# Performance work log

Measured on AMD Instinct MI355X. Metric: run time of the kernel, lower is better.

The kernel has to match this reference:

```python
import jax, jax.numpy as jnp
import numpy as np

B, H, W, C = 16, 64, 64, 256
DIM = 256

def setup_inputs() -> dict:
    key = jax.random.key(0)
    ks = jax.random.split(key, 9)
    s_in = 1.0 / np.sqrt(C)
    x = jax.random.normal(ks[0], (B, H, W, C), dtype=jnp.float32)
    Wq = jax.random.normal(ks[1], (C, DIM), dtype=jnp.float32) * s_in
    bq = jnp.zeros((DIM,), dtype=jnp.float32)
    Wk = jax.random.normal(ks[2], (C, DIM), dtype=jnp.float32) * s_in
    bk = jnp.zeros((DIM,), dtype=jnp.float32)
    Wv = jax.random.normal(ks[3], (C, DIM), dtype=jnp.float32) * s_in
    bv = jnp.zeros((DIM,), dtype=jnp.float32)
    # 'out' conv sees 1 input channel (after the channel reduce_sum)
    Wo = jax.random.normal(ks[4], (1, DIM), dtype=jnp.float32)
    bo = jnp.zeros((DIM,), dtype=jnp.float32)
    return {"x": x, "Wq": Wq, "bq": bq, "Wk": Wk, "bk": bk,
            "Wv": Wv, "bv": bv, "Wo": Wo, "bo": bo}

def reference(x, Wq, bq, Wk, bk, Wv, bv, Wo, bo):
    # 1x1 convs == channel GEMMs
    q = jnp.einsum('bhwc,cd->bhwd', x, Wq) + bq
    k = jnp.einsum('bhwc,cd->bhwd', x, Wk) + bk
    v = jnp.einsum('bhwc,cd->bhwd', x, Wv) + bv
    # channel-reduce score -> [B,H,W,1], softmax jointly over spatial axes
    score = jnp.sum(q * k, axis=-1, keepdims=True)
    attn = jax.nn.softmax(score, axis=(1, 2))
    # channel-reduce of v weighted by per-pixel attn -> [B,H,W,1]
    out = jnp.sum(v * attn, axis=-1, keepdims=True)
    # final 1x1 conv: 1 input channel -> DIM output channels
    return jnp.einsum('bhwc,cd->bhwd', out, Wo) + bo
```

## Files before the change

### kernel.cpp

```cpp
#include <hip/hip_runtime.h>


typedef __bf16 bf16_t;
typedef __attribute__((ext_vector_type(8))) __bf16 bf16x8;
typedef __attribute__((ext_vector_type(4))) float f32x4;

typedef __attribute__((address_space(1))) const unsigned int as1_uint;
typedef __attribute__((address_space(3))) unsigned int as3_uint;

__device__ __forceinline__ void gl16(const void* g, void* l) {
    __builtin_amdgcn_global_load_lds((as1_uint*)g, (as3_uint*)l, 16, 0, 0);
}

#define NBATCH 16
#define NPIX   65536
#define PPB    4096
#define EXP_OFF 48.0f

#define MH_OFF    0u
#define ML_OFF    131072u
#define U_OFF     262144u
#define WV_OFF    263168u
#define SCL_OFF   264192u
#define SCORE_OFF 264448u
#define SV_OFF    526592u
#define BSUM_OFF  788736u

__global__ __launch_bounds__(256) void prep_kernel(
    const float* __restrict__ Wq, const float* __restrict__ bq,
    const float* __restrict__ Wk, const float* __restrict__ bk,
    const float* __restrict__ Wv, const float* __restrict__ bv,
    bf16_t* __restrict__ Mh, bf16_t* __restrict__ Ml,
    float* __restrict__ u, float* __restrict__ wv, float* __restrict__ scl,
    float* __restrict__ bsum)
{
    const int t = threadIdx.x;
    if (blockIdx.x < 256) {
        const int c = blockIdx.x;
        __shared__ __align__(16) float wq_row[256];
        __shared__ __align__(16) float wk_row[256];
        wq_row[t] = Wq[c * 256 + t];
        wk_row[t] = Wk[c * 256 + t];
        __syncthreads();
        const float4* wkt = (const float4*)(Wk + t * 256);
        const float4* wqt = (const float4*)(Wq + t * 256);
        const float4* wq4 = (const float4*)wq_row;
        const float4* wk4 = (const float4*)wk_row;
        float d1 = 0.f, d2 = 0.f;
#pragma unroll 8
        for (int i = 0; i < 64; ++i) {
            float4 a = wq4[i], b = wkt[i];
            d1 += a.x * b.x + a.y * b.y + a.z * b.z + a.w * b.w;
            float4 e = wk4[i], f = wqt[i];
            d2 += e.x * f.x + e.y * f.y + e.z * f.z + e.w * f.w;
        }
        float m = 0.5f * (d1 + d2);
        bf16_t h = (bf16_t)m;
        bf16_t l = (bf16_t)(m - (float)h);
        Mh[c * 256 + t] = h;
        Ml[c * 256 + t] = l;
    } else {
        if (t < NBATCH) bsum[t] = 0.f;
        float uacc = 0.f, wvacc = 0.f;
        const float* wqr = Wq + t * 256;
        const float* wkr = Wk + t * 256;
        const float* wvr = Wv + t * 256;
#pragma unroll 4
        for (int d = 0; d < 256; ++d) {
            uacc += wqr[d] * bk[d] + wkr[d] * bq[d];
            wvacc += wvr[d];
        }
        u[t] = uacc;
        wv[t] = wvacc;
        __shared__ float r1[256], r2[256];
        r1[t] = bq[t] * bk[t];
        r2[t] = bv[t];
        __syncthreads();
        for (int s = 128; s > 0; s >>= 1) {
            if (t < s) { r1[t] += r1[t + s]; r2[t] += r2[t + s]; }
            __syncthreads();
        }
        if (t == 0) { scl[0] = r1[0]; scl[1] = r2[0]; }
    }
}

__device__ __forceinline__ float rowsum16(float v) {
    v += __int_as_float(__builtin_amdgcn_update_dpp(0, __float_as_int(v), 0x118, 0xF, 0xF, true));
    v += __int_as_float(__builtin_amdgcn_update_dpp(0, __float_as_int(v), 0x114, 0xF, 0xF, true));
    v += __int_as_float(__builtin_amdgcn_update_dpp(0, __float_as_int(v), 0x112, 0xF, 0xF, true));
    v += __int_as_float(__builtin_amdgcn_update_dpp(0, __float_as_int(v), 0x111, 0xF, 0xF, true));
    return v;
}

__device__ __forceinline__ bf16x8 cvt8(float4 a0, float4 a1) {
    bf16x8 r;
    r[0] = (bf16_t)a0.x; r[1] = (bf16_t)a0.y; r[2] = (bf16_t)a0.z; r[3] = (bf16_t)a0.w;
    r[4] = (bf16_t)a1.x; r[5] = (bf16_t)a1.y; r[6] = (bf16_t)a1.z; r[7] = (bf16_t)a1.w;
    return r;
}

__global__ __launch_bounds__(256, 2) void score_kernel(
    const float* __restrict__ x,
    const bf16_t* __restrict__ Mh, const bf16_t* __restrict__ Ml,
    const float* __restrict__ u, const float* __restrict__ wvp,
    const float* __restrict__ scl,
    float* __restrict__ score, float* __restrict__ svout,
    float* __restrict__ bsum)
{
    __shared__ __align__(16) float Abuf[4 * 4096];
    __shared__ float redS[4][64], redV[4][64], redT[4][64];

    const int t = threadIdx.x;
    const int lane = t & 63;
    const int wid = t >> 6;
    const int l15 = lane & 15;
    const int lg = lane >> 4;
    const int pix0 = blockIdx.x * 64;
    const int wcol0 = wid * 64;
    const float* xbase = x + (size_t)pix0 * 256;

#pragma unroll
    for (int kt = 0; kt < 4; ++kt) {
        float* buf_ = Abuf + kt * 4096;
        const int k0_ = kt * 64;
#pragma unroll
        for (int c_ = 0; c_ < 4; ++c_) {
            int cc_ = wid * 256 + c_ * 64 + lane;
            int r_ = cc_ >> 4, cp_ = cc_ & 15;
            int g_ = cp_ ^ (r_ & 15);
            gl16(xbase + (size_t)r_ * 256 + k0_ + g_ * 4,
                 buf_ + wid * 1024 + c_ * 256);
        }
    }

    f32x4 acc[4][4];
#pragma unroll
    for (int i = 0; i < 4; ++i)
#pragma unroll
        for (int j = 0; j < 4; ++j)
            acc[i][j] = (f32x4){0.f, 0.f, 0.f, 0.f};

    const int bbase = (wcol0 + l15) * 256 + lg * 8;

    __syncthreads();

#pragma unroll
    for (int kt = 0; kt < 4; ++kt) {
        const float* buf = Abuf + kt * 4096;
        const int k0 = kt * 64;
#pragma unroll
        for (int ks = 0; ks < 2; ++ks) {
            bf16x8 af[4];
#pragma unroll
            for (int rf = 0; rf < 4; ++rf) {
                int row = rf * 16 + l15;
                int g0 = ks * 8 + lg * 2;
                int c0 = g0 ^ (row & 15);
                const float* ap = buf + row * 64;
                float4 a0 = *(const float4*)(ap + c0 * 4);
                float4 a1 = *(const float4*)(ap + (c0 ^ 1) * 4);
                af[rf] = cvt8(a0, a1);
            }
            bf16x8 bh[4], bl[4];
#pragma unroll
            for (int cf = 0; cf < 4; ++cf) {
                int bo = bbase + cf * 4096 + k0 + ks * 32;
                bh[cf] = *(const bf16x8*)(Mh + bo);
                bl[cf] = *(const bf16x8*)(Ml + bo);
            }
#pragma unroll
            for (int rf = 0; rf < 4; ++rf)
#pragma unroll
                for (int cf = 0; cf < 4; ++cf) {
                    acc[rf][cf] = __builtin_amdgcn_mfma_f32_16x16x32_bf16(
                        af[rf], bh[cf], acc[rf][cf], 0, 0, 0);
                    acc[rf][cf] = __builtin_amdgcn_mfma_f32_16x16x32_bf16(
                        af[rf], bl[cf], acc[rf][cf], 0, 0, 0);
                }
        }
    }

    float wvc[4], uc[4];
#pragma unroll
    for (int cf = 0; cf < 4; ++cf) {
        wvc[cf] = wvp[wcol0 + cf * 16 + l15];
        uc[cf] = u[wcol0 + cf * 16 + l15];
    }
    const int jj = l15 >> 2, j3 = l15 & 3;
#pragma unroll
    for (int rf = 0; rf < 4; ++rf) {
#pragma unroll
        for (int r = 0; r < 4; ++r) {
            int row = rf * 16 + lg * 4 + r;
            const float* ep = Abuf + wid * 4096 + row * 64 + j3;
            float s = 0.f, v = 0.f, tp = 0.f;
#pragma unroll
            for (int cf = 0; cf < 4; ++cf) {
                int slot = (cf * 4 + jj) ^ (row & 15);
                float xf = ep[slot * 4];
                float e2 = 2.f * xf - (float)(bf16_t)xf;
                s += e2 * acc[rf][cf][r];
                v += xf * wvc[cf];
                tp += xf * uc[cf];
            }
            s = rowsum16(s);
            v = rowsum16(v);
            tp = rowsum16(tp);
            if (l15 == 15) {
                redS[wid][row] = s;
                redV[wid][row] = v;
                redT[wid][row] = tp;
            }
        }
    }
    __syncthreads();
    if (t < 64) {
        float s = scl[0];
        float v = scl[1];
#pragma unroll
        for (int w = 0; w < 4; ++w) {
            s += redS[w][t] + redT[w][t];
            v += redV[w][t];
        }
        score[pix0 + t] = s;
        svout[pix0 + t] = v;
        float pe = __expf(s - EXP_OFF);
#pragma unroll
        for (int m = 1; m < 64; m <<= 1) pe += __shfl_xor(pe, m, 64);
        if (t == 0) atomicAdd(&bsum[pix0 >> 12], pe);
    }
}

__global__ __launch_bounds__(256) void out_kernel(
    const float* __restrict__ score, const float* __restrict__ sv,
    const float* __restrict__ bsum,
    const float* __restrict__ Wo, const float* __restrict__ bo,
    float* __restrict__ out)
{
    const int total = NPIX * 64;
    const int stride = gridDim.x * blockDim.x;
    for (int idx = blockIdx.x * blockDim.x + threadIdx.x; idx < total; idx += stride) {
        int p = idx >> 6;
        int c4 = (idx & 63) << 2;
        int b = p >> 12;
        float g = __expf(score[p] - EXP_OFF) / bsum[b] * sv[p];
        float4 w = *(const float4*)(Wo + c4);
        float4 bb = *(const float4*)(bo + c4);
        float4 o = { g * w.x + bb.x, g * w.y + bb.y, g * w.z + bb.z, g * w.w + bb.w };
        *(float4*)(out + (size_t)p * 256 + c4) = o;
    }
}

extern "C" void kernel_launch(void* const* d_in, const int* in_sizes, int n_in,
                              void* d_out, int out_size, void* d_ws, size_t ws_size,
                              hipStream_t stream) {
    const float* x  = (const float*)d_in[0];
    const float* Wq = (const float*)d_in[1];
    const float* bq = (const float*)d_in[2];
    const float* Wk = (const float*)d_in[3];
    const float* bk = (const float*)d_in[4];
    const float* Wv = (const float*)d_in[5];
    const float* bv = (const float*)d_in[6];
    const float* Wo = (const float*)d_in[7];
    const float* bo = (const float*)d_in[8];
    float* out = (float*)d_out;
    char* ws = (char*)d_ws;

    bf16_t* Mh = (bf16_t*)(ws + MH_OFF);
    bf16_t* Ml = (bf16_t*)(ws + ML_OFF);
    float* u   = (float*)(ws + U_OFF);
    float* wv  = (float*)(ws + WV_OFF);
    float* scl = (float*)(ws + SCL_OFF);
    float* score = (float*)(ws + SCORE_OFF);
    float* sv    = (float*)(ws + SV_OFF);
    float* bsum  = (float*)(ws + BSUM_OFF);

    prep_kernel<<<dim3(257), dim3(256), 0, stream>>>(Wq, bq, Wk, bk, Wv, bv, Mh, Ml, u, wv, scl, bsum);
    score_kernel<<<dim3(NPIX / 64), dim3(256), 0, stream>>>(x, Mh, Ml, u, wv, scl, score, sv, bsum);
    out_kernel<<<dim3(4096), dim3(256), 0, stream>>>(score, sv, bsum, Wo, bo, out);
}
```

Measured before the change: 107.2 us.

## Fuse score and output kernels via cooperative grid sync

Replaces the separate score and output kernels with one cooperative kernel. Each block handles 64 pixels in two 32-pixel tiles with a smaller LDS footprint so four blocks fit per CU. The block keeps scores and sv values in shared memory, waits on a grid-wide barrier for the per-batch softmax sums, then writes the output directly. This removes the global score/sv round trip and one kernel launch. In exchange it depends on 1024 co-resident blocks and pays for a grid barrier, and it falls back to the old two-kernel path if the cooperative launch fails.

```diff
diff --git a/kernel.cpp b/kernel.cpp
--- a/kernel.cpp
+++ b/kernel.cpp
@@ -1,4 +1,7 @@
 #include <hip/hip_runtime.h>
+#include <hip/hip_cooperative_groups.h>
+
+namespace cg = cooperative_groups;
 
 
 typedef __bf16 bf16_t;
@@ -99,6 +102,162 @@
     return r;
 }
 
+__global__ __launch_bounds__(256, 4) void fused_score_out(
+    const float* __restrict__ x,
+    const bf16_t* __restrict__ Mh, const bf16_t* __restrict__ Ml,
+    const float* __restrict__ u, const float* __restrict__ wvp,
+    const float* __restrict__ scl, float* __restrict__ bsum,
+    const float* __restrict__ Wo, const float* __restrict__ bo,
+    float* __restrict__ out)
+{
+    __shared__ __align__(16) float Abuf[4 * 2048];
+    __shared__ float redS[4][32], redV[4][32], redT[4][32];
+    __shared__ float scoreL[64], svL[64], gL[64];
+
+    const int t = threadIdx.x;
+    const int lane = t & 63;
+    const int wid = t >> 6;
+    const int l15 = lane & 15;
+    const int lg = lane >> 4;
+    const int wcol0 = wid * 64;
+    const int bbase = (wcol0 + l15) * 256 + lg * 8;
+    const int pix0b = blockIdx.x * 64;
+
+    float wvc[4], uc[4];
+#pragma unroll
+    for (int cf = 0; cf < 4; ++cf) {
+        wvc[cf] = wvp[wcol0 + cf * 16 + l15];
+        uc[cf] = u[wcol0 + cf * 16 + l15];
+    }
+    const float c0s = scl[0], bvs = scl[1];
+
+    for (int tt = 0; tt < 2; ++tt) {
+        const int pix0 = pix0b + tt * 32;
+        const float* xbase = x + (size_t)pix0 * 256;
+
+#pragma unroll
+        for (int kt = 0; kt < 4; ++kt) {
+#pragma unroll
+            for (int c_ = 0; c_ < 2; ++c_) {
+                int cc = wid * 128 + c_ * 64 + lane;
+                int r = cc >> 4, cp = cc & 15;
+                int g = cp ^ (r & 15);
+                gl16(xbase + (size_t)r * 256 + kt * 64 + g * 4,
+                     Abuf + kt * 2048 + wid * 512 + c_ * 256);
+            }
+        }
+
+        f32x4 acc[2][4];
+#pragma unroll
+        for (int i = 0; i < 2; ++i)
+#pragma unroll
+            for (int j = 0; j < 4; ++j)
+                acc[i][j] = (f32x4){0.f, 0.f, 0.f, 0.f};
+
+        __syncthreads();
+
+#pragma unroll
+        for (int kt = 0; kt < 4; ++kt) {
+            const float* buf = Abuf + kt * 2048;
+            const int k0 = kt * 64;
+#pragma unroll
+            for (int ks = 0; ks < 2; ++ks) {
+                bf16x8 af[2];
+#pragma unroll
+                for (int rf = 0; rf < 2; ++rf) {
+                    int row = rf * 16 + l15;
+                    int g0 = ks * 8 + lg * 2;
+                    int c0 = g0 ^ (row & 15);
+                    const float* ap = buf + row * 64;
+                    float4 a0 = *(const float4*)(ap + c0 * 4);
+                    float4 a1 = *(const float4*)(ap + (c0 ^ 1) * 4);
+                    af[rf] = cvt8(a0, a1);
+                }
+                bf16x8 bh[4], bl[4];
+#pragma unroll
+                for (int cf = 0; cf < 4; ++cf) {
+                    int boff = bbase + cf * 4096 + k0 + ks * 32;
+                    bh[cf] = *(const bf16x8*)(Mh + boff);
+                    bl[cf] = *(const bf16x8*)(Ml + boff);
+                }
+#pragma unroll
+                for (int rf = 0; rf < 2; ++rf)
+#pragma unroll
+                    for (int cf = 0; cf < 4; ++cf) {
+                        acc[rf][cf] = __builtin_amdgcn_mfma_f32_16x16x32_bf16(
+                            af[rf], bh[cf], acc[rf][cf], 0, 0, 0);
+                        acc[rf][cf] = __builtin_amdgcn_mfma_f32_16x16x32_bf16(
+                            af[rf], bl[cf], acc[rf][cf], 0, 0, 0);
+                    }
+            }
+        }
+
+        const int jj = l15 >> 2, j3 = l15 & 3;
+#pragma unroll
+        for (int rf = 0; rf < 2; ++rf) {
+#pragma unroll
+            for (int r = 0; r < 4; ++r) {
+                int row = rf * 16 + lg * 4 + r;
+                const float* ep = Abuf + wid * 2048 + row * 64 + j3;
+                float s = 0.f, v = 0.f, tp = 0.f;
+#pragma unroll
+                for (int cf = 0; cf < 4; ++cf) {
+                    int slot = (cf * 4 + jj) ^ (row & 15);
+                    float xf = ep[slot * 4];
+                    float e2 = 2.f * xf - (float)(bf16_t)xf;
+                    s += e2 * acc[rf][cf][r];
+                    v += xf * wvc[cf];
+                    tp += xf * uc[cf];
+                }
+                s = rowsum16(s);
+                v = rowsum16(v);
+                tp = rowsum16(tp);
+                if (l15 == 15) {
+                    redS[wid][row] = s;
+                    redV[wid][row] = v;
+                    redT[wid][row] = tp;
+                }
+            }
+        }
+        __syncthreads();
+        if (t < 32) {
+            float s = c0s, v = bvs;
+#pragma unroll
+            for (int w = 0; w < 4; ++w) {
+                s += redS[w][t] + redT[w][t];
+                v += redV[w][t];
+            }
+            scoreL[tt * 32 + t] = s;
+            svL[tt * 32 + t] = v;
+            float pe = __expf(s - EXP_OFF);
+#pragma unroll
+            for (int m = 1; m < 32; m <<= 1) pe += __shfl_xor(pe, m, 64);
+            if (t == 0) atomicAdd(&bsum[pix0b >> 12], pe);
+        }
+    }
+
+    cg::this_grid().sync();
+
+    const int b = pix0b >> 12;
+    if (t < 64) {
+        float Z = __hip_atomic_load(&bsum[b], __ATOMIC_RELAXED, __HIP_MEMORY_SCOPE_AGENT);
+        gL[t] = __expf(scoreL[t] - EXP_OFF) / Z * svL[t];
+    }
+    __syncthreads();
+    const int c4 = (t & 63) << 2;
+    float4 w4 = *(const float4*)(Wo + c4);
+    float4 b4 = *(const float4*)(bo + c4);
+    float* obase = out + (size_t)pix0b * 256 + c4;
+#pragma unroll
+    for (int i = 0; i < 16; ++i) {
+        int p = i * 4 + wid;
+        float g = gL[p];
+        float4 o = { g * w4.x + b4.x, g * w4.y + b4.y,
+                     g * w4.z + b4.z, g * w4.w + b4.w };
+        *(float4*)(obase + (size_t)p * 256) = o;
+    }
+}
+
 __global__ __launch_bounds__(256, 2) void score_kernel(
     const float* __restrict__ x,
     const bf16_t* __restrict__ Mh, const bf16_t* __restrict__ Ml,
@@ -141,7 +300,6 @@
             acc[i][j] = (f32x4){0.f, 0.f, 0.f, 0.f};
 
     const int bbase = (wcol0 + l15) * 256 + lg * 8;
-
     __syncthreads();
 
 #pragma unroll
@@ -164,9 +322,9 @@
             bf16x8 bh[4], bl[4];
 #pragma unroll
             for (int cf = 0; cf < 4; ++cf) {
-                int bo = bbase + cf * 4096 + k0 + ks * 32;
-                bh[cf] = *(const bf16x8*)(Mh + bo);
-                bl[cf] = *(const bf16x8*)(Ml + bo);
+                int boff = bbase + cf * 4096 + k0 + ks * 32;
+                bh[cf] = *(const bf16x8*)(Mh + boff);
+                bl[cf] = *(const bf16x8*)(Ml + boff);
             }
 #pragma unroll
             for (int rf = 0; rf < 4; ++rf)
@@ -266,16 +424,28 @@
     float* out = (float*)d_out;
     char* ws = (char*)d_ws;
 
-    bf16_t* Mh = (bf16_t*)(ws + MH_OFF);
-    bf16_t* Ml = (bf16_t*)(ws + ML_OFF);
-    float* u   = (float*)(ws + U_OFF);
-    float* wv  = (float*)(ws + WV_OFF);
-    float* scl = (float*)(ws + SCL_OFF);
+    const bf16_t* Mh = (const bf16_t*)(ws + MH_OFF);
+    const bf16_t* Ml = (const bf16_t*)(ws + ML_OFF);
+    const float* u   = (const float*)(ws + U_OFF);
+    const float* wv  = (const float*)(ws + WV_OFF);
+    const float* scl = (const float*)(ws + SCL_OFF);
     float* score = (float*)(ws + SCORE_OFF);
     float* sv    = (float*)(ws + SV_OFF);
     float* bsum  = (float*)(ws + BSUM_OFF);
 
-    prep_kernel<<<dim3(257), dim3(256), 0, stream>>>(Wq, bq, Wk, bk, Wv, bv, Mh, Ml, u, wv, scl, bsum);
-    score_kernel<<<dim3(NPIX / 64), dim3(256), 0, stream>>>(x, Mh, Ml, u, wv, scl, score, sv, bsum);
-    out_kernel<<<dim3(4096), dim3(256), 0, stream>>>(score, sv, bsum, Wo, bo, out);
-}
+    prep_kernel<<<dim3(257), dim3(256), 0, stream>>>(
+        Wq, bq, Wk, bk, Wv, bv,
+        (bf16_t*)(ws + MH_OFF), (bf16_t*)(ws + ML_OFF),
+        (float*)(ws + U_OFF), (float*)(ws + WV_OFF), (float*)(ws + SCL_OFF), bsum);
+
+    void* args[] = { (void*)&x, (void*)&Mh, (void*)&Ml, (void*)&u, (void*)&wv,
+                     (void*)&scl, (void*)&bsum, (void*)&Wo, (void*)&bo, (void*)&out };
+    hipError_t err = hipLaunchCooperativeKernel(
+        (const void*)fused_score_out, dim3(1024), dim3(256), args, 0, stream);
+
+    if (err != hipSuccess) {
+        score_kernel<<<dim3(NPIX / 64), dim3(256), 0, stream>>>(
+            x, Mh, Ml, u, wv, scl, score, sv, bsum);
+        out_kernel<<<dim3(4096), dim3(256), 0, stream>>>(score, sv, bsum, Wo, bo, out);
+    }
+}
```

Result: slower. 381.5 us (+256.0%).
